# Kernel tuning notes

Hardware: AMD Instinct MI355X
Metric: run time of the kernel (lower is better)

## Reference

```python
import jax, jax.numpy as jnp
import numpy as np

NX, NY = 512, 512
FNUM, GNUM = 120, 120
NA = 1.35
WAVELENGTH = NX * NA / 100.0  # chosen so normalized period = 100
N_LIQUID = 1.44
M_RED = 0.25
LOW_LIGHT_THRES = 1e-3
SRC_STEEP = 8.0
RESIST_STEEP = 30.0
RESIST_INT = 0.225
DOSES = (0.98, 1.0, 1.02)
SRC_GRID = 13

X1 = NX // 2 - FNUM; X2 = NX // 2 + FNUM + 1
Y1 = NY // 2 - GNUM; Y2 = NY // 2 + GNUM + 1
_PER_X = NX / (WAVELENGTH / NA)
_PER_Y = NY / (WAVELENGTH / NA)
NORM_SPEC = _PER_X * _PER_Y
DFMDG = 1.0 / NORM_SPEC
_fm = (np.arange(X1, X2) - NX // 2) / _PER_X
_gm = (np.arange(Y1, Y2) - NY // 2) / _PER_Y
_FM, _GM = np.meshgrid(_fm, _gm)  # 'xy' indexing, shape [2*GNUM+1, 2*FNUM+1]
FM = jnp.asarray(_FM, jnp.float32)
GM = jnp.asarray(_GM, jnp.float32)


def cal_pupil(fg2):
    # obliquity factor; pupil phase is identically zero in this module
    num = 1.0 - (M_RED ** 2) * (NA ** 2) * fg2
    den = 1.0 - (NA / N_LIQUID) ** 2 * fg2
    return jnp.sqrt(jnp.sqrt(num / den))


def setup_inputs() -> dict:
    key = jax.random.key(0)
    g = np.linspace(-1.0, 1.0, SRC_GRID, dtype=np.float32)
    fxg, fyg = np.meshgrid(g, g)
    r = np.sqrt(fxg ** 2 + fyg ** 2)
    data = ((r >= 0.6) & (r <= 0.9)).astype(np.float32)  # annular source
    # sigmoid activation init: +1 where lit, -1 elsewhere (zeros, set 2 where data>0.5, sub 1)
    params = 2.0 * data - 1.0
    mask_value = jax.random.uniform(key, (NY, NX), jnp.float32)
    return {
        "mask_value": mask_value,
        "source_params": jnp.asarray(params, jnp.float32),
        "source_fx": jnp.asarray(fxg.reshape(-1), jnp.float32),
        "source_fy": jnp.asarray(fyg.reshape(-1), jnp.float32),
    }


def _forward(mask_value, source_params, source_fx, source_fy):
    # source activation + low-light pruning (masked_select expressed as zero-weighting)
    val = jax.nn.sigmoid(SRC_STEEP * source_params).reshape(-1)  # [S]
    valid = val >= LOW_LIGHT_THRES
    w = jnp.where(valid, val, 0.0)
    weight = jnp.sum(w)

    # normalization intensity (detached in the original)
    fxy2 = source_fx ** 2 + source_fy ** 2
    obl = cal_pupil(jnp.where(valid, fxy2, 0.0))
    norm_I = jax.lax.stop_gradient(
        N_LIQUID * DFMDG ** 2 * jnp.sum(w * (NORM_SPEC * obl) ** 2) / weight
    )

    # shifted pupil per source point over the mask frequency window
    F = FM[None, :, :] + source_fx[:, None, None]  # [S, Gy, Gx]
    G = GM[None, :, :] + source_fy[:, None, None]
    rho2 = F * F + G * G                            # == mask_fg2m + 2(fx*fm+fy*gm) + fxy2
    vmask = rho2 <= 1.0
    pupil = jnp.where(vmask, cal_pupil(jnp.where(vmask, rho2, 0.0)), 0.0)  # [S, Gy, Gx]

    S = w.shape[0]
    Is, Rs = [], []
    for d in DOSES:
        fv = jnp.fft.fftshift(jnp.fft.fft2(jnp.fft.ifftshift(mask_value * d)))
        win = fv[Y1:Y2, X1:X2]                      # [Gy, Gx] complex
        tempH = win[None, :, :] * pupil.astype(jnp.complex64)  # masked spectrum*pupil
        e = jnp.zeros((S, NY, NX), jnp.complex64).at[:, Y1:Y2, X1:X2].set(tempH)
        AA = jnp.fft.fftshift(jnp.fft.ifft2(e), axes=(-2, -1))
        I2 = AA.real ** 2 + AA.imag ** 2            # |AA * conj(AA)|
        intensity = jnp.einsum('s,syx->yx', w, I2) / weight / norm_I
        Is.append(intensity)
        Rs.append(jax.nn.sigmoid(RESIST_STEEP * (intensity - RESIST_INT)))
    # [2, 3, NY, NX]: [0] = aerial intensity per dose, [1] = resist image per dose
    return jnp.stack([jnp.stack(Is), jnp.stack(Rs)])


def reference(mask_value, source_params, source_fx, source_fy):
    return _forward(mask_value, source_params, source_fx, source_fy)
```

## Files before the change

### kernel.cpp

```cpp
#include <hip/hip_runtime.h>
#include <hip/hip_bf16.h>


#define SPLIT 4

static const size_t O_TW   = 4096;
static const size_t O_ACC  = 8192;
static const size_t ACC_BYTES = (size_t)SPLIT * 512 * 512 * 4;
static const size_t O_WIN  = O_ACC + ACC_BYTES;
static const size_t O_R1   = O_WIN + 464896;
static const size_t O_T2   = O_R1 + 987136;
static const size_t SLOT_BYTES = (size_t)512 * 244 * 8;

__device__ inline float2 cadd(float2 a, float2 b){ return make_float2(a.x+b.x, a.y+b.y); }
__device__ inline float2 csub(float2 a, float2 b){ return make_float2(a.x-b.x, a.y-b.y); }
__device__ inline float2 cmul(float2 a, float2 b){
  return make_float2(fmaf(a.x, b.x, -(a.y*b.y)), fmaf(a.x, b.y, a.y*b.x));
}
__device__ inline float2 twsgn(float2 t, int S) {
  return make_float2(t.x, (S > 0) ? t.y : -t.y);
}

template<int S>
__device__ inline void dft8(float2 v[8]) {
  const float sg = (float)S;
  const float C7 = 0.7071067811865476f;
  float2 t0=cadd(v[0],v[4]), t4=csub(v[0],v[4]);
  float2 t1=cadd(v[1],v[5]), t5=csub(v[1],v[5]);
  float2 t2=cadd(v[2],v[6]), t6=csub(v[2],v[6]);
  float2 t3=cadd(v[3],v[7]), t7=csub(v[3],v[7]);
  t5 = make_float2(C7*(t5.x - sg*t5.y), C7*(t5.y + sg*t5.x));
  t6 = make_float2(-sg*t6.y, sg*t6.x);
  t7 = make_float2(C7*(-t7.x - sg*t7.y), C7*(sg*t7.x - t7.y));
  float2 u0=cadd(t0,t2), u2=csub(t0,t2);
  float2 u1=cadd(t1,t3), u3=csub(t1,t3);
  u3 = make_float2(-sg*u3.y, sg*u3.x);
  float2 u4=cadd(t4,t6), u6=csub(t4,t6);
  float2 u5=cadd(t5,t7), u7=csub(t5,t7);
  u7 = make_float2(-sg*u7.y, sg*u7.x);
  v[0]=cadd(u0,u1); v[4]=csub(u0,u1);
  v[2]=cadd(u2,u3); v[6]=csub(u2,u3);
  v[1]=cadd(u4,u5); v[5]=csub(u4,u5);
  v[3]=cadd(u6,u7); v[7]=csub(u6,u7);
}

template<int S>
__device__ inline void wfft512(float2 v[8], int lane, float2* xch,
                               const float2* twt) {
  const int p2 = lane & 7, u0 = lane >> 3;
  dft8<S>(v);
  { float2 t1 = twsgn(twt[lane], S), acc = t1;
    v[1] = cmul(v[1], acc);
    #pragma unroll
    for (int u = 2; u < 8; u++) { acc = cmul(acc, t1); v[u] = cmul(v[u], acc); } }
  __builtin_amdgcn_wave_barrier();
  #pragma unroll
  for (int u = 0; u < 8; u++) xch[u*68 + p2*8 + u0] = v[u];
  __builtin_amdgcn_wave_barrier();
  { const float4* rp = (const float4*)(xch + u0*68 + p2*8);
    #pragma unroll
    for (int q = 0; q < 4; q++) {
      float4 t = rp[q];
      v[2*q]   = make_float2(t.x, t.y);
      v[2*q+1] = make_float2(t.z, t.w);
    } }
  dft8<S>(v);
  { float2 t1 = twsgn(twt[p2 << 3], S), acc = t1;
    v[1] = cmul(v[1], acc);
    #pragma unroll
    for (int u = 2; u < 8; u++) { acc = cmul(acc, t1); v[u] = cmul(v[u], acc); } }
  __builtin_amdgcn_wave_barrier();
  #pragma unroll
  for (int u = 0; u < 8; u++) xch[u*68 + lane] = v[u];
  __builtin_amdgcn_wave_barrier();
  { const float4* rp = (const float4*)(xch + p2*68 + u0*8);
    #pragma unroll
    for (int q = 0; q < 4; q++) {
      float4 t = rp[q];
      v[2*q]   = make_float2(t.x, t.y);
      v[2*q+1] = make_float2(t.z, t.w);
    } }
  dft8<S>(v);
}

__global__ void __launch_bounds__(256) k_setup(const float* prm, const float* sfx,
                                               const float* sfy, char* ws) {
  __shared__ float sw[169], sx[169], sy[169];
  __shared__ double so[169];
  int t = threadIdx.x;
  if (t < 169) {
    float p = prm[t];
    float val = 1.f / (1.f + __expf(-8.f * p));
    float w = (val >= 0.001f) ? val : 0.f;
    double o = 0.0; float fx = 0.f, fy = 0.f;
    if (w > 0.f) {
      fx = sfx[t]; fy = sfy[t];
      double f2 = (double)fx*(double)fx + (double)fy*(double)fy;
      o = (double)w * sqrt((1.0 - 0.11390625 * f2) / (1.0 - 0.87890625 * f2));
    }
    sw[t] = w; so[t] = o; sx[t] = fx; sy[t] = fy;
  }
  float2* gtw = (float2*)(ws + O_TW);
  for (int k = t; k < 512; k += 256) {
    double a = 6.283185307179586476925286766559 * (double)k / 512.0;
    gtw[k] = make_float2((float)cos(a), (float)sin(a));
  }
  if (t < 241) ((float*)ws)[768 + t] = (float)(((double)(t - 120)) / 100.0);
  __syncthreads();
  if (t == 0) {
    float* wsf = (float*)ws; int* wsi = (int*)ws;
    double Sden = 0.0; int c = 0;
    for (int s = 0; s < 169; s++) {
      Sden += so[s];
      if (sw[s] > 0.f) { wsf[64+c] = sw[s]; wsf[320+c] = sx[s]; wsf[576+c] = sy[s]; c++; }
    }
    wsi[0] = c;
    wsf[1] = (float)(1.0 / (68719476736.0 * 1.44 * Sden));
  }
}

__global__ void __launch_bounds__(256, 6) k_b1(const float* mask, const char* wsb,
                                               float2* R1t) {
  int lane = threadIdx.x & 63, wv = threadIdx.x >> 6;
  int y = blockIdx.x * 4 + wv;
  __shared__ __align__(16) float2 lds[4*544];
  __shared__ __align__(16) float2 twt[512];
  ((float4*)twt)[threadIdx.x] = ((const float4*)(wsb + O_TW))[threadIdx.x];
  __syncthreads();
  float2 v[8];
  #pragma unroll
  for (int q = 0; q < 8; q++) v[q] = make_float2(mask[y*512 + 64*q + lane], 0.f);
  wfft512<-1>(v, lane, lds + wv*544, twt);
  #pragma unroll
  for (int u = 0; u < 8; u++) {
    int k = (lane>>3) + 8*(lane&7) + 64*u;
    int beta = (k >= 392) ? (k - 392) : ((k <= 120) ? (k + 120) : -1);
    if (beta >= 0) R1t[beta*512 + y] = v[u];
  }
}

__global__ void __launch_bounds__(256, 6) k_b2(const float2* R1t, const char* wsb,
                                               float2* Wg) {
  int lane = threadIdx.x & 63, wv = threadIdx.x >> 6;
  int j = blockIdx.x * 4 + wv;
  __shared__ __align__(16) float2 lds[4*544];
  __shared__ __align__(16) float2 twt[512];
  ((float4*)twt)[threadIdx.x] = ((const float4*)(wsb + O_TW))[threadIdx.x];
  __syncthreads();
  float2 v[8];
  #pragma unroll
  for (int q = 0; q < 8; q++)
    v[q] = (j < 241) ? R1t[j*512 + 64*q + lane] : make_float2(0.f, 0.f);
  wfft512<-1>(v, lane, lds + wv*544, twt);
  if (j < 241) {
    #pragma unroll
    for (int u = 0; u < 8; u++) {
      int k = (lane>>3) + 8*(lane&7) + 64*u;
      int alpha = (k >= 392) ? (k - 392) : ((k <= 120) ? (k + 120) : -1);
      if (alpha >= 0) Wg[alpha*241 + j] = v[u];
    }
  }
}

__global__ void __launch_bounds__(256, 6) k_c1(const float2* Wg, const char* wsb,
                                               int base, float2* T2) {
  const int*   cnt = (const int*)wsb;
  const float* wsf = (const float*)wsb;
  const float* FMt = (const float*)(wsb + 3072);
  int sic  = blockIdx.x / 31;
  int tile = blockIdx.x % 31;
  int slot = base + sic;
  if (slot >= *cnt) return;
  __shared__ __align__(16) float2 lds[4*544];
  __shared__ __align__(16) float2 twt[512];
  ((float4*)twt)[threadIdx.x] = ((const float4*)(wsb + O_TW))[threadIdx.x];
  __syncthreads();
  float fx = wsf[320 + slot], fy = wsf[576 + slot];
  int lane = threadIdx.x & 63, wv = threadIdx.x >> 6;
  float2* xch = lds + wv*544;
  #pragma unroll
  for (int ph = 0; ph < 2; ph++) {
    int alpha = tile*8 + ph*4 + wv;
    bool arow = (alpha < 241);
    float Gf = __fadd_rn(arow ? FMt[alpha] : 0.f, fy);
    float g2 = __fmul_rn(Gf, Gf);
    float2 v[8];
    #pragma unroll
    for (int q = 0; q < 8; q++) {
      int n = 64*q + lane;
      float2 val = make_float2(0.f, 0.f);
      if (arow && n < 241) {
        float Ff = __fadd_rn(FMt[n], fx);
        float r2 = __fadd_rn(__fmul_rn(Ff, Ff), g2);
        if (r2 <= 1.0f) {
          float num = fmaf(-0.11390625f, r2, 1.0f);
          float den = fmaf(-0.87890625f, r2, 1.0f);
          float P = __fsqrt_rn(__fsqrt_rn(__fdividef(num, den)));
          float2 Wv = Wg[alpha*241 + n];
          val = make_float2(P * Wv.x, P * Wv.y);
        }
      }
      v[q] = val;
    }
    wfft512<1>(v, lane, xch, twt);
    #pragma unroll
    for (int u = 0; u < 8; u++) {
      int xx = (lane>>3) + 8*(lane&7) + 64*u;
      xch[xx] = v[u];
    }
    __syncthreads();
    int colb = tile*8 + ph*4;
    if (colb < 244) {
      #pragma unroll
      for (int r = 0; r < 2; r++) {
        int x = (int)threadIdx.x + 256*r;
        float2 a0 = lds[0*544+x], a1 = lds[1*544+x];
        float2 a2 = lds[2*544+x], a3 = lds[3*544+x];
        float4* dst = (float4*)(T2 + ((size_t)sic*512 + x)*244 + colb);
        dst[0] = make_float4(a0.x, a0.y, a1.x, a1.y);
        dst[1] = make_float4(a2.x, a2.y, a3.x, a3.y);
      }
    }
    __syncthreads();
  }
}

__global__ void __launch_bounds__(64, 4) k_c2(const float2* T2, const char* wsb,
                                              int base, int CH, int first,
                                              float* accbuf) {
  const int*   cnt = (const int*)wsb;
  const float* wsf = (const float*)wsb;
  int x    = blockIdx.x >> 2;
  int part = blockIdx.x & 3;
  int lane = threadIdx.x;
  __shared__ __align__(16) float2 xch[544];
  __shared__ __align__(16) float2 twt[512];
  #pragma unroll
  for (int i = 0; i < 4; i++)
    ((float4*)twt)[lane + 64*i] = ((const float4*)(wsb + O_TW))[lane + 64*i];
  __builtin_amdgcn_wave_barrier();
  int count = *cnt;
  float av[8] = {0.f,0.f,0.f,0.f,0.f,0.f,0.f,0.f};
  bool touched = false;
  int sic = part;
  bool act = (sic < CH) && (base + sic < count);
  float2 pv[4] = {{0.f,0.f},{0.f,0.f},{0.f,0.f},{0.f,0.f}};
  if (act) {
    const float2* row = T2 + ((size_t)sic*512 + x)*244;
    #pragma unroll
    for (int q = 0; q < 4; q++) {
      int n = 64*q + lane;
      pv[q] = (n < 241) ? row[n] : make_float2(0.f, 0.f);
    }
  }
  while (act) {
    float w = wsf[64 + base + sic];
    float2 v[8];
    #pragma unroll
    for (int q = 0; q < 4; q++) v[q] = pv[q];
    #pragma unroll
    for (int q = 4; q < 8; q++) v[q] = make_float2(0.f, 0.f);
    int nsic = sic + SPLIT;
    act = (nsic < CH) && (base + nsic < count);
    if (act) {
      const float2* row = T2 + ((size_t)nsic*512 + x)*244;
      #pragma unroll
      for (int q = 0; q < 4; q++) {
        int n = 64*q + lane;
        pv[q] = (n < 241) ? row[n] : make_float2(0.f, 0.f);
      }
    }
    wfft512<1>(v, lane, xch, twt);
    #pragma unroll
    for (int u = 0; u < 8; u++)
      av[u] = fmaf(w, fmaf(v[u].x, v[u].x, v[u].y*v[u].y), av[u]);
    touched = true;
    sic = nsic;
  }
  float* a = accbuf + ((size_t)part << 18) + (size_t)x * 512;
  int y0 = (lane>>3) + 8*(lane&7);
  if (first) {
    #pragma unroll
    for (int u = 0; u < 8; u++) a[y0 + 64*u] = av[u];
  } else if (touched) {
    #pragma unroll
    for (int u = 0; u < 8; u++) a[y0 + 64*u] += av[u];
  }
}

__global__ void __launch_bounds__(256) k_final(const float* acc, const char* wsb,
                                               float* out) {
  __shared__ float tile[64][65];
  const float* wsf = (const float*)wsb;
  float scale = wsf[1];
  int x0 = (blockIdx.x & 7) * 64, y0 = (blockIdx.x >> 3) * 64;
  int j = threadIdx.x & 63, i0 = threadIdx.x >> 6;
  #pragma unroll
  for (int k = 0; k < 16; k++) {
    int i = i0 + 4*k;
    const float* ap = acc + (size_t)(x0 + i)*512 + y0 + j;
    tile[i][j] = ap[0] + ap[1<<18] + ap[2<<18] + ap[3<<18];
  }
  __syncthreads();
  const float dd[3] = {0.9604f, 1.0f, 1.0404f};
  #pragma unroll
  for (int k = 0; k < 16; k++) {
    int yy = i0 + 4*k;
    float I = scale * tile[j][yy];
    int o = (y0 + yy)*512 + x0 + j;
    #pragma unroll
    for (int d = 0; d < 3; d++) {
      float Ik = dd[d] * I;
      out[(size_t)d*262144 + o] = Ik;
      out[(size_t)(3+d)*262144 + o] = 1.f / (1.f + __expf(-30.f*(Ik - 0.225f)));
    }
  }
}

extern "C" void kernel_launch(void* const* d_in, const int* in_sizes, int n_in,
                              void* d_out, int out_size, void* d_ws, size_t ws_size,
                              hipStream_t stream) {
  (void)in_sizes; (void)n_in; (void)out_size;
  const float* mask = (const float*)d_in[0];
  const float* prm  = (const float*)d_in[1];
  const float* sfx  = (const float*)d_in[2];
  const float* sfy  = (const float*)d_in[3];
  float* out = (float*)d_out;
  char*  ws  = (char*)d_ws;

  float*  acc = (float*)(ws + O_ACC);
  float2* Wg  = (float2*)(ws + O_WIN);
  float2* R1t = (float2*)(ws + O_R1);
  float2* T2  = (float2*)(ws + O_T2);

  k_setup<<<dim3(1),   dim3(256), 0, stream>>>(prm, sfx, sfy, ws);
  k_b1  <<<dim3(128), dim3(256), 0, stream>>>(mask, (const char*)ws, R1t);
  k_b2  <<<dim3(61),  dim3(256), 0, stream>>>(R1t, (const char*)ws, Wg);

  size_t avail = (ws_size > O_T2) ? (ws_size - O_T2) : 0;
  int CH = (int)(avail / SLOT_BYTES);
  if (CH > 169) CH = 169;
  if (CH < 1)   CH = 1;
  for (int base = 0; base < 169; base += CH) {
    k_c1<<<dim3((unsigned)(CH*31)), dim3(256), 0, stream>>>(Wg, (const char*)ws, base, T2);
    k_c2<<<dim3(512*SPLIT),         dim3(64),  0, stream>>>(T2, (const char*)ws, base, CH,
                                                            (base == 0) ? 1 : 0, acc);
  }
  k_final<<<dim3(64), dim3(256), 0, stream>>>(acc, (const char*)ws, out);
}
```

Before: 153.6 us.

## Store intermediate column FFTs in fp16, skip zero half in final FFT, widen split

The intermediate T2 buffer between the column and row inverse FFTs is now stored as half2 instead of float2. Values are prescaled by 1/512 before storage to stay in fp16 range, and the normalization constant is adjusted to match. The final FFT's first radix-8 stage skips its known-zero upper half inputs. The accumulation split grows from 4 to 8, with more workgroups per CU. Together these halve the memory traffic on the dominant intermediate, let more source points fit per chunk, and increase parallelism, at the cost of fp16 rounding error in the aerial image and a larger accumulator reduction. The ACC_BYTES size now scales with SPLIT=8, which shifts the other workspace offsets.

```diff
diff --git a/kernel.cpp b/kernel.cpp
--- a/kernel.cpp
+++ b/kernel.cpp
@@ -1,8 +1,9 @@
 #include <hip/hip_runtime.h>
 #include <hip/hip_bf16.h>
-
-
-#define SPLIT 4
+#include <hip/hip_fp16.h>
+
+
+#define SPLIT 8
 
 static const size_t O_TW   = 4096;
 static const size_t O_ACC  = 8192;
@@ -10,7 +11,7 @@
 static const size_t O_WIN  = O_ACC + ACC_BYTES;
 static const size_t O_R1   = O_WIN + 464896;
 static const size_t O_T2   = O_R1 + 987136;
-static const size_t SLOT_BYTES = (size_t)512 * 244 * 8;
+static const size_t SLOT_BYTES = (size_t)512 * 244 * 4;
 
 __device__ inline float2 cadd(float2 a, float2 b){ return make_float2(a.x+b.x, a.y+b.y); }
 __device__ inline float2 csub(float2 a, float2 b){ return make_float2(a.x-b.x, a.y-b.y); }
@@ -21,14 +22,22 @@
   return make_float2(t.x, (S > 0) ? t.y : -t.y);
 }
 
-template<int S>
+template<int S, bool ZTOP>
 __device__ inline void dft8(float2 v[8]) {
   const float sg = (float)S;
   const float C7 = 0.7071067811865476f;
-  float2 t0=cadd(v[0],v[4]), t4=csub(v[0],v[4]);
-  float2 t1=cadd(v[1],v[5]), t5=csub(v[1],v[5]);
-  float2 t2=cadd(v[2],v[6]), t6=csub(v[2],v[6]);
-  float2 t3=cadd(v[3],v[7]), t7=csub(v[3],v[7]);
+  float2 t0, t1, t2, t3, t4, t5, t6, t7;
+  if (ZTOP) {
+    t0 = v[0]; t4 = v[0];
+    t1 = v[1]; t5 = v[1];
+    t2 = v[2]; t6 = v[2];
+    t3 = v[3]; t7 = v[3];
+  } else {
+    t0=cadd(v[0],v[4]); t4=csub(v[0],v[4]);
+    t1=cadd(v[1],v[5]); t5=csub(v[1],v[5]);
+    t2=cadd(v[2],v[6]); t6=csub(v[2],v[6]);
+    t3=cadd(v[3],v[7]); t7=csub(v[3],v[7]);
+  }
   t5 = make_float2(C7*(t5.x - sg*t5.y), C7*(t5.y + sg*t5.x));
   t6 = make_float2(-sg*t6.y, sg*t6.x);
   t7 = make_float2(C7*(-t7.x - sg*t7.y), C7*(sg*t7.x - t7.y));
@@ -44,11 +53,11 @@
   v[3]=cadd(u6,u7); v[7]=csub(u6,u7);
 }
 
-template<int S>
+template<int S, bool ZTOP>
 __device__ inline void wfft512(float2 v[8], int lane, float2* xch,
                                const float2* twt) {
   const int p2 = lane & 7, u0 = lane >> 3;
-  dft8<S>(v);
+  dft8<S, ZTOP>(v);
   { float2 t1 = twsgn(twt[lane], S), acc = t1;
     v[1] = cmul(v[1], acc);
     #pragma unroll
@@ -64,7 +73,7 @@
       v[2*q]   = make_float2(t.x, t.y);
       v[2*q+1] = make_float2(t.z, t.w);
     } }
-  dft8<S>(v);
+  dft8<S, false>(v);
   { float2 t1 = twsgn(twt[p2 << 3], S), acc = t1;
     v[1] = cmul(v[1], acc);
     #pragma unroll
@@ -80,7 +89,7 @@
       v[2*q]   = make_float2(t.x, t.y);
       v[2*q+1] = make_float2(t.z, t.w);
     } }
-  dft8<S>(v);
+  dft8<S, false>(v);
 }
 
 __global__ void __launch_bounds__(256) k_setup(const float* prm, const float* sfx,
@@ -115,7 +124,7 @@
       if (sw[s] > 0.f) { wsf[64+c] = sw[s]; wsf[320+c] = sx[s]; wsf[576+c] = sy[s]; c++; }
     }
     wsi[0] = c;
-    wsf[1] = (float)(1.0 / (68719476736.0 * 1.44 * Sden));
+    wsf[1] = (float)(1.0 / (262144.0 * 1.44 * Sden));
   }
 }
 
@@ -130,7 +139,7 @@
   float2 v[8];
   #pragma unroll
   for (int q = 0; q < 8; q++) v[q] = make_float2(mask[y*512 + 64*q + lane], 0.f);
-  wfft512<-1>(v, lane, lds + wv*544, twt);
+  wfft512<-1, false>(v, lane, lds + wv*544, twt);
   #pragma unroll
   for (int u = 0; u < 8; u++) {
     int k = (lane>>3) + 8*(lane&7) + 64*u;
@@ -151,7 +160,7 @@
   #pragma unroll
   for (int q = 0; q < 8; q++)
     v[q] = (j < 241) ? R1t[j*512 + 64*q + lane] : make_float2(0.f, 0.f);
-  wfft512<-1>(v, lane, lds + wv*544, twt);
+  wfft512<-1, false>(v, lane, lds + wv*544, twt);
   if (j < 241) {
     #pragma unroll
     for (int u = 0; u < 8; u++) {
@@ -162,8 +171,8 @@
   }
 }
 
-__global__ void __launch_bounds__(256, 6) k_c1(const float2* Wg, const char* wsb,
-                                               int base, float2* T2) {
+__global__ void __launch_bounds__(256, 7) k_c1(const float2* Wg, const char* wsb,
+                                               int base, __half2* T2) {
   const int*   cnt = (const int*)wsb;
   const float* wsf = (const float*)wsb;
   const float* FMt = (const float*)(wsb + 3072);
@@ -195,14 +204,15 @@
         if (r2 <= 1.0f) {
           float num = fmaf(-0.11390625f, r2, 1.0f);
           float den = fmaf(-0.87890625f, r2, 1.0f);
-          float P = __fsqrt_rn(__fsqrt_rn(__fdividef(num, den)));
+          float P = __fsqrt_rn(__fsqrt_rn(__fdividef(num, den)))
+                    * 0.001953125f;
           float2 Wv = Wg[alpha*241 + n];
           val = make_float2(P * Wv.x, P * Wv.y);
         }
       }
       v[q] = val;
     }
-    wfft512<1>(v, lane, xch, twt);
+    wfft512<1, false>(v, lane, xch, twt);
     #pragma unroll
     for (int u = 0; u < 8; u++) {
       int xx = (lane>>3) + 8*(lane&7) + 64*u;
@@ -214,24 +224,26 @@
       #pragma unroll
       for (int r = 0; r < 2; r++) {
         int x = (int)threadIdx.x + 256*r;
-        float2 a0 = lds[0*544+x], a1 = lds[1*544+x];
-        float2 a2 = lds[2*544+x], a3 = lds[3*544+x];
-        float4* dst = (float4*)(T2 + ((size_t)sic*512 + x)*244 + colb);
-        dst[0] = make_float4(a0.x, a0.y, a1.x, a1.y);
-        dst[1] = make_float4(a2.x, a2.y, a3.x, a3.y);
+        union { __half2 h[4]; float4 f; } u;
+        #pragma unroll
+        for (int wvi = 0; wvi < 4; wvi++) {
+          float2 a = lds[wvi*544 + x];
+          u.h[wvi] = __floats2half2_rn(a.x, a.y);
+        }
+        *(float4*)(T2 + ((size_t)sic*512 + x)*244 + colb) = u.f;
       }
     }
     __syncthreads();
   }
 }
 
-__global__ void __launch_bounds__(64, 4) k_c2(const float2* T2, const char* wsb,
+__global__ void __launch_bounds__(64, 8) k_c2(const __half2* T2, const char* wsb,
                                               int base, int CH, int first,
                                               float* accbuf) {
   const int*   cnt = (const int*)wsb;
   const float* wsf = (const float*)wsb;
-  int x    = blockIdx.x >> 2;
-  int part = blockIdx.x & 3;
+  int x    = blockIdx.x >> 3;
+  int part = blockIdx.x & (SPLIT-1);
   int lane = threadIdx.x;
   __shared__ __align__(16) float2 xch[544];
   __shared__ __align__(16) float2 twt[512];
@@ -241,40 +253,38 @@
   __builtin_amdgcn_wave_barrier();
   int count = *cnt;
   float av[8] = {0.f,0.f,0.f,0.f,0.f,0.f,0.f,0.f};
-  bool touched = false;
   int sic = part;
   bool act = (sic < CH) && (base + sic < count);
-  float2 pv[4] = {{0.f,0.f},{0.f,0.f},{0.f,0.f},{0.f,0.f}};
+  __half2 pv[4] = {{0.f,0.f},{0.f,0.f},{0.f,0.f},{0.f,0.f}};
   if (act) {
-    const float2* row = T2 + ((size_t)sic*512 + x)*244;
+    const __half2* row = T2 + ((size_t)sic*512 + x)*244;
     #pragma unroll
     for (int q = 0; q < 4; q++) {
       int n = 64*q + lane;
-      pv[q] = (n < 241) ? row[n] : make_float2(0.f, 0.f);
+      pv[q] = (n < 241) ? row[n] : __half2{0.f, 0.f};
     }
   }
   while (act) {
     float w = wsf[64 + base + sic];
     float2 v[8];
     #pragma unroll
-    for (int q = 0; q < 4; q++) v[q] = pv[q];
+    for (int q = 0; q < 4; q++) { float2 f = __half22float2(pv[q]); v[q] = f; }
     #pragma unroll
     for (int q = 4; q < 8; q++) v[q] = make_float2(0.f, 0.f);
     int nsic = sic + SPLIT;
     act = (nsic < CH) && (base + nsic < count);
     if (act) {
-      const float2* row = T2 + ((size_t)nsic*512 + x)*244;
+      const __half2* row = T2 + ((size_t)nsic*512 + x)*244;
       #pragma unroll
       for (int q = 0; q < 4; q++) {
         int n = 64*q + lane;
-        pv[q] = (n < 241) ? row[n] : make_float2(0.f, 0.f);
+        pv[q] = (n < 241) ? row[n] : __half2{0.f, 0.f};
       }
     }
-    wfft512<1>(v, lane, xch, twt);
+    wfft512<1, true>(v, lane, xch, twt);
     #pragma unroll
     for (int u = 0; u < 8; u++)
       av[u] = fmaf(w, fmaf(v[u].x, v[u].x, v[u].y*v[u].y), av[u]);
-    touched = true;
     sic = nsic;
   }
   float* a = accbuf + ((size_t)part << 18) + (size_t)x * 512;
@@ -282,7 +292,7 @@
   if (first) {
     #pragma unroll
     for (int u = 0; u < 8; u++) a[y0 + 64*u] = av[u];
-  } else if (touched) {
+  } else {
     #pragma unroll
     for (int u = 0; u < 8; u++) a[y0 + 64*u] += av[u];
   }
@@ -299,7 +309,10 @@
   for (int k = 0; k < 16; k++) {
     int i = i0 + 4*k;
     const float* ap = acc + (size_t)(x0 + i)*512 + y0 + j;
-    tile[i][j] = ap[0] + ap[1<<18] + ap[2<<18] + ap[3<<18];
+    float s = 0.f;
+    #pragma unroll
+    for (int p = 0; p < SPLIT; p++) s += ap[(size_t)p << 18];
+    tile[i][j] = s;
   }
   __syncthreads();
   const float dd[3] = {0.9604f, 1.0f, 1.0404f};
@@ -328,10 +341,10 @@
   float* out = (float*)d_out;
   char*  ws  = (char*)d_ws;
 
-  float*  acc = (float*)(ws + O_ACC);
-  float2* Wg  = (float2*)(ws + O_WIN);
-  float2* R1t = (float2*)(ws + O_R1);
-  float2* T2  = (float2*)(ws + O_T2);
+  float*   acc = (float*)(ws + O_ACC);
+  float2*  Wg  = (float2*)(ws + O_WIN);
+  float2*  R1t = (float2*)(ws + O_R1);
+  __half2* T2  = (__half2*)(ws + O_T2);
 
   k_setup<<<dim3(1),   dim3(256), 0, stream>>>(prm, sfx, sfy, ws);
   k_b1  <<<dim3(128), dim3(256), 0, stream>>>(mask, (const char*)ws, R1t);
```

After: 147.4 us. 4.1% less time.
